# Performance work log

Hardware: AMD Instinct MI355X
Metric: run time of the kernel (lower is better)

## Reference

```python
import jax, jax.numpy as jnp
import numpy as np

STRIDE = 1
PAD = 3
DIL = 1


def setup_inputs() -> dict:
    key = jax.random.key(0)
    k1, k2, k3 = jax.random.split(key, 3)
    B, C, H, W = 8, 256, 64, 64
    G, K = 4, 7
    Ho, Wo = 64, 64  # same-padding, stride 1
    return {
        "input": jax.random.normal(k1, (B, C, H, W), dtype=jnp.float32),
        "weight": jax.random.normal(k2, (B, G, K, K, Ho, Wo), dtype=jnp.float32),
        "bias": jax.random.normal(k3, (C,), dtype=jnp.float32),
    }


def reference(input, weight, bias):
    # input: [B,C,H,W], weight: [B,G,Kh,Kw,Ho,Wo], bias: [C]
    B, C, H, W = input.shape
    G, Kh, Kw, Ho, Wo = weight.shape[1:]
    Cpg = C // G
    xp = jnp.pad(input, ((0, 0), (0, 0), (PAD, PAD), (PAD, PAD)))
    # group view: [B, G, C/G, H+2p, W+2p]
    xg = xp.reshape(B, G, Cpg, H + 2 * PAD, W + 2 * PAD)
    out = jnp.zeros((B, G, Cpg, Ho, Wo), dtype=input.dtype)
    # fused accumulation over the K*K kernel taps; no im2col blowup
    for kh in range(Kh):
        for kw in range(Kw):
            h0 = kh * DIL
            w0 = kw * DIL
            patch = xg[:, :, :, h0:h0 + Ho * STRIDE:STRIDE, w0:w0 + Wo * STRIDE:STRIDE]
            out = out + patch * weight[:, :, kh, kw][:, :, None, :, :]
    out = out.reshape(B, C, Ho, Wo) + bias[None, :, None, None]
    return out
```

## Files before the change

kernel.cpp:

```cpp
#include <hip/hip_runtime.h>


#define BLK_X 16
#define BLK_Y 16
#define NTHR (BLK_X * BLK_Y)
#define NC 4
#define TILE_Y 16
#define STG_ROWS (TILE_Y + 6)
#define STG_COLS 70
#define LDS_STRIDE 71
#define STG_N (NC * STG_ROWS * STG_COLS)
#define NSTG ((STG_N + NTHR - 1) / NTHR)

__global__ __launch_bounds__(NTHR, 4)
void involution_kernel(const float* __restrict__ in,
                       const float* __restrict__ w,
                       const float* __restrict__ bias,
                       float* __restrict__ out) {
    __shared__ float lds[NC * STG_ROWS * LDS_STRIDE];

    const int tx = threadIdx.x;
    const int ty = threadIdx.y;
    const int tid = ty * BLK_X + tx;
    const int x0 = tx * 4;
    const int Y0 = blockIdx.x * TILE_Y;
    const int y  = Y0 + ty;
    const int c0 = blockIdx.y * NC;
    const int bz = blockIdx.z;
    const int g  = bz & 3;

    const float* inb = in + (size_t)bz * 64 * 4096 + (size_t)c0 * 4096;

    #pragma unroll
    for (int j = 0; j < NSTG; ++j) {
        int i = tid + j * NTHR;
        if (i < STG_N) {
            int ci  = i / (STG_ROWS * STG_COLS);
            int rem = i - ci * (STG_ROWS * STG_COLS);
            int rr  = rem / STG_COLS;
            int cc  = rem - rr * STG_COLS;
            int gy  = Y0 + rr - 3;
            int gx  = cc - 3;
            float v = 0.f;
            if (gy >= 0 && gy < 64 && gx >= 0 && gx < 64)
                v = inb[ci * 4096 + gy * 64 + gx];
            lds[(ci * STG_ROWS + rr) * LDS_STRIDE + cc] = v;
        }
    }
    __syncthreads();

    float acc[NC][4];
    #pragma unroll
    for (int ci = 0; ci < NC; ++ci) {
        acc[ci][0] = 0.f; acc[ci][1] = 0.f; acc[ci][2] = 0.f; acc[ci][3] = 0.f;
    }

    const float* wb = w + (size_t)bz * 49 * 4096 + y * 64 + x0;

    #pragma unroll 1
    for (int kh = 0; kh < 7; ++kh) {
        float4 wr[7];
        #pragma unroll
        for (int kw = 0; kw < 7; ++kw)
            wr[kw] = *(const float4*)(wb + (size_t)(kh * 7 + kw) * 4096);

        #pragma unroll
        for (int ci = 0; ci < NC; ++ci) {
            const float* lr = &lds[(ci * STG_ROWS + ty + kh) * LDS_STRIDE + x0];
            float v[10];
            #pragma unroll
            for (int j = 0; j < 10; ++j) v[j] = lr[j];
            #pragma unroll
            for (int kw = 0; kw < 7; ++kw) {
                acc[ci][0] += v[kw + 0] * wr[kw].x;
                acc[ci][1] += v[kw + 1] * wr[kw].y;
                acc[ci][2] += v[kw + 2] * wr[kw].z;
                acc[ci][3] += v[kw + 3] * wr[kw].w;
            }
        }
    }

    float* outb = out + (size_t)bz * 64 * 4096 + (size_t)c0 * 4096 + y * 64 + x0;
    #pragma unroll
    for (int ci = 0; ci < NC; ++ci) {
        const float bv = bias[g * 64 + c0 + ci];
        float4 o;
        o.x = acc[ci][0] + bv; o.y = acc[ci][1] + bv;
        o.z = acc[ci][2] + bv; o.w = acc[ci][3] + bv;
        *(float4*)(outb + (size_t)ci * 4096) = o;
    }
}

extern "C" void kernel_launch(void* const* d_in, const int* in_sizes, int n_in,
                              void* d_out, int out_size, void* d_ws, size_t ws_size,
                              hipStream_t stream) {
    const float* in   = (const float*)d_in[0];
    const float* wgt  = (const float*)d_in[1];
    const float* bias = (const float*)d_in[2];
    float* out = (float*)d_out;

    dim3 block(BLK_X, BLK_Y, 1);
    dim3 grid(64 / TILE_Y, 64 / NC, 32);
    involution_kernel<<<grid, block, 0, stream>>>(in, wgt, bias, out);
}
```

Before: 134.2 us.

## Widen per-thread output to 8 pixels, double-buffer weight rows, column-wise LDS staging

Each thread now computes 8 horizontal outputs per channel instead of 4, which halves the block to 128 threads and reuses LDS row reads across more outputs. Weight rows for the next kh are loaded into a second register buffer while the current row is computed, so global loads overlap with FMAs. The LDS fill is restructured so only 70 threads each stage one column across rows and channels, removing the div/mod index math. In exchange, register pressure rises (8x4 accumulators plus two 14-float4 weight buffers), occupancy hints drop, and the staging phase is serialized over fewer threads.

```diff
diff --git a/kernel.cpp b/kernel.cpp
--- a/kernel.cpp
+++ b/kernel.cpp
@@ -1,18 +1,15 @@
 #include <hip/hip_runtime.h>
 
 
-#define BLK_X 16
-#define BLK_Y 16
-#define NTHR (BLK_X * BLK_Y)
+#define TX 8
+#define TYB 16
+#define NTHR (TX * TYB)
 #define NC 4
-#define TILE_Y 16
-#define STG_ROWS (TILE_Y + 6)
+#define STG_ROWS 22
 #define STG_COLS 70
 #define LDS_STRIDE 71
-#define STG_N (NC * STG_ROWS * STG_COLS)
-#define NSTG ((STG_N + NTHR - 1) / NTHR)
 
-__global__ __launch_bounds__(NTHR, 4)
+__global__ __launch_bounds__(NTHR, 2)
 void involution_kernel(const float* __restrict__ in,
                        const float* __restrict__ w,
                        const float* __restrict__ bias,
@@ -21,9 +18,9 @@
 
     const int tx = threadIdx.x;
     const int ty = threadIdx.y;
-    const int tid = ty * BLK_X + tx;
-    const int x0 = tx * 4;
-    const int Y0 = blockIdx.x * TILE_Y;
+    const int tid = ty * TX + tx;
+    const int x0 = tx * 8;
+    const int Y0 = blockIdx.x * TYB;
     const int y  = Y0 + ty;
     const int c0 = blockIdx.y * NC;
     const int bz = blockIdx.z;
@@ -31,63 +28,85 @@
 
     const float* inb = in + (size_t)bz * 64 * 4096 + (size_t)c0 * 4096;
 
-    #pragma unroll
-    for (int j = 0; j < NSTG; ++j) {
-        int i = tid + j * NTHR;
-        if (i < STG_N) {
-            int ci  = i / (STG_ROWS * STG_COLS);
-            int rem = i - ci * (STG_ROWS * STG_COLS);
-            int rr  = rem / STG_COLS;
-            int cc  = rem - rr * STG_COLS;
-            int gy  = Y0 + rr - 3;
-            int gx  = cc - 3;
-            float v = 0.f;
-            if (gy >= 0 && gy < 64 && gx >= 0 && gx < 64)
-                v = inb[ci * 4096 + gy * 64 + gx];
-            lds[(ci * STG_ROWS + rr) * LDS_STRIDE + cc] = v;
+    if (tid < STG_COLS) {
+        const int col = tid;
+        const int gx  = col - 3;
+        const bool xok = (gx >= 0) && (gx < 64);
+        #pragma unroll 1
+        for (int ci = 0; ci < NC; ++ci) {
+            const float* p  = inb + ci * 4096 + gx;
+            float*       lp = &lds[ci * STG_ROWS * LDS_STRIDE + col];
+            #pragma unroll
+            for (int rr = 0; rr < STG_ROWS; ++rr) {
+                int gy = Y0 + rr - 3;
+                float v = 0.f;
+                if (xok && gy >= 0 && gy < 64) v = p[gy * 64];
+                lp[rr * LDS_STRIDE] = v;
+            }
         }
     }
     __syncthreads();
 
-    float acc[NC][4];
+    float acc[NC][8];
     #pragma unroll
-    for (int ci = 0; ci < NC; ++ci) {
-        acc[ci][0] = 0.f; acc[ci][1] = 0.f; acc[ci][2] = 0.f; acc[ci][3] = 0.f;
-    }
+    for (int ci = 0; ci < NC; ++ci)
+        #pragma unroll
+        for (int e = 0; e < 8; ++e) acc[ci][e] = 0.f;
 
     const float* wb = w + (size_t)bz * 49 * 4096 + y * 64 + x0;
 
-    #pragma unroll 1
-    for (int kh = 0; kh < 7; ++kh) {
-        float4 wr[7];
+    float4 W0[2][7], W1[2][7];
+
+    auto loadrow = [&](int kh, float4 (&W)[2][7]) {
         #pragma unroll
-        for (int kw = 0; kw < 7; ++kw)
-            wr[kw] = *(const float4*)(wb + (size_t)(kh * 7 + kw) * 4096);
-
+        for (int kw = 0; kw < 7; ++kw) {
+            const float* p = wb + (size_t)(kh * 7 + kw) * 4096;
+            W[0][kw] = *(const float4*)p;
+            W[1][kw] = *(const float4*)(p + 4);
+        }
+    };
+    auto comprow = [&](int kh, const float4 (&W)[2][7]) {
         #pragma unroll
         for (int ci = 0; ci < NC; ++ci) {
             const float* lr = &lds[(ci * STG_ROWS + ty + kh) * LDS_STRIDE + x0];
-            float v[10];
+            float v[14];
             #pragma unroll
-            for (int j = 0; j < 10; ++j) v[j] = lr[j];
+            for (int j = 0; j < 14; ++j) v[j] = lr[j];
             #pragma unroll
             for (int kw = 0; kw < 7; ++kw) {
-                acc[ci][0] += v[kw + 0] * wr[kw].x;
-                acc[ci][1] += v[kw + 1] * wr[kw].y;
-                acc[ci][2] += v[kw + 2] * wr[kw].z;
-                acc[ci][3] += v[kw + 3] * wr[kw].w;
+                #pragma unroll
+                for (int q = 0; q < 2; ++q) {
+                    const float4 wv = W[q][kw];
+                    acc[ci][q * 4 + 0] += v[4 * q + 0 + kw] * wv.x;
+                    acc[ci][q * 4 + 1] += v[4 * q + 1 + kw] * wv.y;
+                    acc[ci][q * 4 + 2] += v[4 * q + 2 + kw] * wv.z;
+                    acc[ci][q * 4 + 3] += v[4 * q + 3 + kw] * wv.w;
+                }
             }
         }
+    };
+
+    loadrow(0, W0);
+    #pragma unroll 1
+    for (int kh = 0; kh < 6; kh += 2) {
+        loadrow(kh + 1, W1);
+        comprow(kh, W0);
+        loadrow(kh + 2, W0);
+        comprow(kh + 1, W1);
     }
+    comprow(6, W0);
 
     float* outb = out + (size_t)bz * 64 * 4096 + (size_t)c0 * 4096 + y * 64 + x0;
     #pragma unroll
     for (int ci = 0; ci < NC; ++ci) {
         const float bv = bias[g * 64 + c0 + ci];
-        float4 o;
-        o.x = acc[ci][0] + bv; o.y = acc[ci][1] + bv;
-        o.z = acc[ci][2] + bv; o.w = acc[ci][3] + bv;
-        *(float4*)(outb + (size_t)ci * 4096) = o;
+        float4 o0, o1;
+        o0.x = acc[ci][0] + bv; o0.y = acc[ci][1] + bv;
+        o0.z = acc[ci][2] + bv; o0.w = acc[ci][3] + bv;
+        o1.x = acc[ci][4] + bv; o1.y = acc[ci][5] + bv;
+        o1.z = acc[ci][6] + bv; o1.w = acc[ci][7] + bv;
+        *(float4*)(outb + (size_t)ci * 4096)     = o0;
+        *(float4*)(outb + (size_t)ci * 4096 + 4) = o1;
     }
 }
 
@@ -99,7 +118,7 @@
     const float* bias = (const float*)d_in[2];
     float* out = (float*)d_out;
 
-    dim3 block(BLK_X, BLK_Y, 1);
-    dim3 grid(64 / TILE_Y, 64 / NC, 32);
+    dim3 block(TX, TYB, 1);
+    dim3 grid(64 / TYB, 64 / NC, 32);
     involution_kernel<<<grid, block, 0, stream>>>(in, wgt, bias, out);
 }
```

After: 177.5 us. +32.3%, slower.

## Keep per-pixel weights in registers and loop channels with prefetched LDS staging

Applied to the files above, without the earlier changes.

Restructures the kernel so each thread holds its 7x7 per-pixel weights in registers (split across two half-waves by kernel rows) and loops over 32 channels per block. The next channel's input tile is prefetched into registers while the current one is computed, and the two half-wave partial sums are combined with a cross-lane shuffle. This removes repeated weight reloads from global memory across channel blocks. The cost is a large register footprint, two barriers per channel, and a smaller grid of 128-thread blocks.

```diff
diff --git a/kernel.cpp b/kernel.cpp
--- a/kernel.cpp
+++ b/kernel.cpp
@@ -1,93 +1,123 @@
 #include <hip/hip_runtime.h>
 
 
-#define BLK_X 16
-#define BLK_Y 16
-#define NTHR (BLK_X * BLK_Y)
-#define NC 4
-#define TILE_Y 16
-#define STG_ROWS (TILE_Y + 6)
+#define NTHR 128
+#define TILE_Y 4
+#define NCH 32
+#define STG_ROWS 10
 #define STG_COLS 70
 #define LDS_STRIDE 71
-#define STG_N (NC * STG_ROWS * STG_COLS)
+#define STG_N (STG_ROWS * STG_COLS)
 #define NSTG ((STG_N + NTHR - 1) / NTHR)
 
-__global__ __launch_bounds__(NTHR, 4)
+__global__ __launch_bounds__(NTHR, 2)
 void involution_kernel(const float* __restrict__ in,
                        const float* __restrict__ w,
                        const float* __restrict__ bias,
                        float* __restrict__ out) {
-    __shared__ float lds[NC * STG_ROWS * LDS_STRIDE];
+    __shared__ float lds[STG_ROWS * LDS_STRIDE];
 
-    const int tx = threadIdx.x;
-    const int ty = threadIdx.y;
-    const int tid = ty * BLK_X + tx;
-    const int x0 = tx * 4;
-    const int Y0 = blockIdx.x * TILE_Y;
-    const int y  = Y0 + ty;
-    const int c0 = blockIdx.y * NC;
-    const int bz = blockIdx.z;
-    const int g  = bz & 3;
+    const int tid  = threadIdx.x;
+    const int lane = tid & 63;
+    const int wv   = tid >> 6;
+    const int half = lane >> 5;
+    const int sub  = lane & 31;
+    const int q    = sub & 15;
+    const int r    = (sub >> 4) | (wv << 1);
+    const int x0   = q * 4;
+    const int Y0   = blockIdx.x * TILE_Y;
+    const int y    = Y0 + r;
+    const int c0   = blockIdx.y * NCH;
+    const int bz   = blockIdx.z;
+    const int g    = bz & 3;
+    const int khb  = half ? 3 : 0;
 
-    const float* inb = in + (size_t)bz * 64 * 4096 + (size_t)c0 * 4096;
+    float4 W[28];
+    const float* wb = w + (size_t)bz * 49 * 4096 + y * 64 + x0;
+    #pragma unroll
+    for (int k = 0; k < 28; ++k) {
+        const int kh = khb + k / 7;
+        const int kw = k % 7;
+        float4 v = make_float4(0.f, 0.f, 0.f, 0.f);
+        if (half == 0 || k >= 7)
+            v = *(const float4*)(wb + (size_t)(kh * 7 + kw) * 4096);
+        W[k] = v;
+    }
+
+    int goff[NSTG];
+    int laddr[NSTG];
+    #pragma unroll
+    for (int j = 0; j < NSTG; ++j) {
+        const int i = tid + j * NTHR;
+        goff[j] = -1; laddr[j] = -1;
+        if (i < STG_N) {
+            const int rr = i / STG_COLS;
+            const int cc = i - rr * STG_COLS;
+            laddr[j] = rr * LDS_STRIDE + cc;
+            const int gy = Y0 + rr - 3;
+            const int gx = cc - 3;
+            if (gy >= 0 && gy < 64 && gx >= 0 && gx < 64)
+                goff[j] = gy * 64 + gx;
+        }
+    }
+
+    const float* inb  = in  + (size_t)bz * 64 * 4096 + (size_t)c0 * 4096;
+    float*       outb = out + (size_t)bz * 64 * 4096 + (size_t)c0 * 4096 + y * 64 + x0;
+    const float* bias_g = bias + g * 64 + c0;
 
     #pragma unroll
     for (int j = 0; j < NSTG; ++j) {
-        int i = tid + j * NTHR;
-        if (i < STG_N) {
-            int ci  = i / (STG_ROWS * STG_COLS);
-            int rem = i - ci * (STG_ROWS * STG_COLS);
-            int rr  = rem / STG_COLS;
-            int cc  = rem - rr * STG_COLS;
-            int gy  = Y0 + rr - 3;
-            int gx  = cc - 3;
-            float v = 0.f;
-            if (gy >= 0 && gy < 64 && gx >= 0 && gx < 64)
-                v = inb[ci * 4096 + gy * 64 + gx];
-            lds[(ci * STG_ROWS + rr) * LDS_STRIDE + cc] = v;
-        }
+        if (laddr[j] >= 0)
+            lds[laddr[j]] = (goff[j] >= 0) ? inb[goff[j]] : 0.f;
     }
     __syncthreads();
 
-    float acc[NC][4];
-    #pragma unroll
-    for (int ci = 0; ci < NC; ++ci) {
-        acc[ci][0] = 0.f; acc[ci][1] = 0.f; acc[ci][2] = 0.f; acc[ci][3] = 0.f;
-    }
+    #pragma unroll 1
+    for (int c = 0; c < NCH; ++c) {
+        float pf[NSTG];
+        const float* pc = inb + (size_t)(c + 1) * 4096;
+        if (c + 1 < NCH) {
+            #pragma unroll
+            for (int j = 0; j < NSTG; ++j)
+                pf[j] = (goff[j] >= 0) ? pc[goff[j]] : 0.f;
+        }
 
-    const float* wb = w + (size_t)bz * 49 * 4096 + y * 64 + x0;
-
-    #pragma unroll 1
-    for (int kh = 0; kh < 7; ++kh) {
-        float4 wr[7];
+        float acc0 = 0.f, acc1 = 0.f, acc2 = 0.f, acc3 = 0.f;
         #pragma unroll
-        for (int kw = 0; kw < 7; ++kw)
-            wr[kw] = *(const float4*)(wb + (size_t)(kh * 7 + kw) * 4096);
-
-        #pragma unroll
-        for (int ci = 0; ci < NC; ++ci) {
-            const float* lr = &lds[(ci * STG_ROWS + ty + kh) * LDS_STRIDE + x0];
+        for (int j = 0; j < 4; ++j) {
+            const float* lr = &lds[(r + khb + j) * LDS_STRIDE + x0];
             float v[10];
             #pragma unroll
-            for (int j = 0; j < 10; ++j) v[j] = lr[j];
+            for (int d = 0; d < 10; ++d) v[d] = lr[d];
             #pragma unroll
             for (int kw = 0; kw < 7; ++kw) {
-                acc[ci][0] += v[kw + 0] * wr[kw].x;
-                acc[ci][1] += v[kw + 1] * wr[kw].y;
-                acc[ci][2] += v[kw + 2] * wr[kw].z;
-                acc[ci][3] += v[kw + 3] * wr[kw].w;
+                const float4 wv4 = W[j * 7 + kw];
+                acc0 += v[kw + 0] * wv4.x;
+                acc1 += v[kw + 1] * wv4.y;
+                acc2 += v[kw + 2] * wv4.z;
+                acc3 += v[kw + 3] * wv4.w;
             }
         }
-    }
 
-    float* outb = out + (size_t)bz * 64 * 4096 + (size_t)c0 * 4096 + y * 64 + x0;
-    #pragma unroll
-    for (int ci = 0; ci < NC; ++ci) {
-        const float bv = bias[g * 64 + c0 + ci];
-        float4 o;
-        o.x = acc[ci][0] + bv; o.y = acc[ci][1] + bv;
-        o.z = acc[ci][2] + bv; o.w = acc[ci][3] + bv;
-        *(float4*)(outb + (size_t)ci * 4096) = o;
+        acc0 += __shfl_xor(acc0, 32);
+        acc1 += __shfl_xor(acc1, 32);
+        acc2 += __shfl_xor(acc2, 32);
+        acc3 += __shfl_xor(acc3, 32);
+
+        const float bv = bias_g[c];
+        if (half == 0) {
+            float4 o;
+            o.x = acc0 + bv; o.y = acc1 + bv; o.z = acc2 + bv; o.w = acc3 + bv;
+            *(float4*)(outb + (size_t)c * 4096) = o;
+        }
+
+        if (c + 1 < NCH) {
+            __syncthreads();
+            #pragma unroll
+            for (int j = 0; j < NSTG; ++j)
+                if (laddr[j] >= 0) lds[laddr[j]] = pf[j];
+            __syncthreads();
+        }
     }
 }
 
@@ -99,7 +129,7 @@
     const float* bias = (const float*)d_in[2];
     float* out = (float*)d_out;
 
-    dim3 block(BLK_X, BLK_Y, 1);
-    dim3 grid(64 / TILE_Y, 64 / NC, 32);
+    dim3 block(NTHR, 1, 1);
+    dim3 grid(64 / TILE_Y, 64 / NCH, 32);
     involution_kernel<<<grid, block, 0, stream>>>(in, wgt, bias, out);
 }
```

Measured after the change: 130.8 us. 1.03x faster.
